# Kernel optimization log

Measured on AMD Instinct MI355X. Metric: run time of the kernel, lower is better.

Reference implementation:

```python
import jax, jax.numpy as jnp
import numpy as np

BATCH, INPUT_DIM, BOND_DIM, OUTPUT_DIM = 4096, 1024, 32, 512


def setup_inputs() -> dict:
    key = jax.random.key(0)
    k1, k2, k3 = jax.random.split(key, 3)
    # inputs centered at 1 so the length-1024 chain product stays O(1) in fp32
    inputs = 1.0 + 0.05 * jax.random.normal(k1, (BATCH, INPUT_DIM), dtype=jnp.float32)
    # cores scaled ~ glorot so each [bond,bond] step roughly preserves norm
    cores = jax.random.normal(k2, (INPUT_DIM, BOND_DIM, BOND_DIM), dtype=jnp.float32) / jnp.sqrt(jnp.float32(BOND_DIM))
    projection = jax.random.normal(k3, (BOND_DIM, OUTPUT_DIM), dtype=jnp.float32) * 0.05
    bias = jnp.zeros((OUTPUT_DIM,), dtype=jnp.float32)
    return {"inputs": inputs, "cores": cores, "projection": projection, "bias": bias}


def reference(inputs, cores, projection, bias):
    # MPS chain: boundary_{i+1}[b,k] = sum_j boundary_i[b,j] * x_i[b] * core_i[j,k]
    batch = inputs.shape[0]
    bond = cores.shape[1]
    boundary0 = jnp.ones((batch, bond), dtype=inputs.dtype)

    def step(boundary, xc):
        x_i, core_i = xc  # x_i: [batch], core_i: [bond, bond]
        new_boundary = (boundary * x_i[:, None]) @ core_i  # [batch, bond]
        return new_boundary, None

    xs = (inputs.T, cores)  # scan over input_dim axis
    final_boundary, _ = jax.lax.scan(step, boundary0, xs)
    return final_boundary @ projection + bias
```

## Files before the change

kernel.cpp:

```cpp
#include <hip/hip_runtime.h>


__device__ __forceinline__ void mm32(const float* __restrict__ A,
                                     const float* __restrict__ B,
                                     float* __restrict__ C, int tid) {
    const int j = tid >> 3;
    const int kq = tid & 7;
    float a[32];
    const float4* __restrict__ A4 = (const float4*)(A + j * 32);
#pragma unroll
    for (int t = 0; t < 8; ++t) {
        float4 v = A4[t];
        a[4 * t + 0] = v.x; a[4 * t + 1] = v.y;
        a[4 * t + 2] = v.z; a[4 * t + 3] = v.w;
    }
    const float4* __restrict__ B4 = (const float4*)B;
    float4 acc0 = make_float4(0.f, 0.f, 0.f, 0.f);
    float4 acc1 = make_float4(0.f, 0.f, 0.f, 0.f);
#pragma unroll
    for (int m = 0; m < 16; ++m) {
        float4 b0 = B4[m * 8 + kq];
        float4 b1 = B4[(m + 16) * 8 + kq];
        acc0.x = fmaf(a[m], b0.x, acc0.x);
        acc0.y = fmaf(a[m], b0.y, acc0.y);
        acc0.z = fmaf(a[m], b0.z, acc0.z);
        acc0.w = fmaf(a[m], b0.w, acc0.w);
        acc1.x = fmaf(a[m + 16], b1.x, acc1.x);
        acc1.y = fmaf(a[m + 16], b1.y, acc1.y);
        acc1.z = fmaf(a[m + 16], b1.z, acc1.z);
        acc1.w = fmaf(a[m + 16], b1.w, acc1.w);
    }
    float4 acc;
    acc.x = acc0.x + acc1.x; acc.y = acc0.y + acc1.y;
    acc.z = acc0.z + acc1.z; acc.w = acc0.w + acc1.w;
    ((float4*)(C + j * 32))[kq] = acc;
}

__global__ __launch_bounds__(256) void k1(const float* __restrict__ cores,
                                          const float* __restrict__ inputs,
                                          float* __restrict__ l1,
                                          float* __restrict__ p) {
    __shared__ __align__(16) float c[4 * 1024];
    __shared__ __align__(16) float ping[1024];
    __shared__ __align__(16) float pong[1024];
    const int tid = threadIdx.x;
    const int s = blockIdx.x;
    const int lane = tid & 63;
    const int wid = tid >> 6;

    const float4* src = (const float4*)(cores + (size_t)s * 4096);
    float4* cd = (float4*)c;
#pragma unroll
    for (int t = 0; t < 4; ++t) cd[tid + 256 * t] = src[tid + 256 * t];

    float prs[4];
#pragma unroll
    for (int rr = 0; rr < 4; ++rr) {
        const int row = s * 16 + wid * 4 + rr;
        const float4* in4 = (const float4*)(inputs + (size_t)row * 1024);
        float4 x0 = in4[lane];
        float4 x1 = in4[lane + 64];
        float4 x2 = in4[lane + 128];
        float4 x3 = in4[lane + 192];
        prs[rr] = ((x0.x * x0.y) * (x0.z * x0.w)) * ((x1.x * x1.y) * (x1.z * x1.w)) *
                  ((x2.x * x2.y) * (x2.z * x2.w)) * ((x3.x * x3.y) * (x3.z * x3.w));
    }
#pragma unroll
    for (int rr = 0; rr < 4; ++rr) {
        float pr = prs[rr];
#pragma unroll
        for (int msk = 1; msk < 64; msk <<= 1) pr *= __shfl_xor(pr, msk);
        if (lane == 0) p[s * 16 + wid * 4 + rr] = pr;
    }

    __syncthreads();
    mm32(c, c + 1024, ping, tid);
    __syncthreads();
    mm32(ping, c + 2048, pong, tid);
    __syncthreads();
    mm32(pong, c + 3072, ping, tid);
    __syncthreads();
    ((float4*)(l1 + (size_t)s * 1024))[tid] = ((const float4*)ping)[tid];
}

__global__ __launch_bounds__(256) void k2b(const float* __restrict__ l1,
                                           float* __restrict__ l2big) {
    __shared__ __align__(16) float m[16 * 1024];
    __shared__ __align__(16) float ping[1024];
    __shared__ __align__(16) float pong[1024];
    const int tid = threadIdx.x;
    const int s = blockIdx.x;
    const int seg = s & 15;
    const float4* src = (const float4*)(l1 + (size_t)seg * 16384);
    float4* md = (float4*)m;
#pragma unroll
    for (int t = 0; t < 16; ++t) md[tid + 256 * t] = src[tid + 256 * t];
    __syncthreads();
    mm32(m, m + 1024, ping, tid);
    __syncthreads();
    float* A = ping;
    float* C = pong;
    for (int t = 2; t < 16; ++t) {
        mm32(A, m + t * 1024, C, tid);
        __syncthreads();
        float* tmp = A; A = C; C = tmp;
    }
    ((float4*)(l2big + (size_t)s * 1024))[tid] = ((const float4*)A)[tid];
}

__global__ __launch_bounds__(256) void k4(const float* __restrict__ l2,
                                          const float* __restrict__ proj,
                                          const float* __restrict__ p,
                                          const float* __restrict__ bias,
                                          float* __restrict__ out) {
    __shared__ __align__(16) float M[16 * 1024];
    __shared__ __align__(16) float qL[512];
    __shared__ __align__(16) float bL[512];
    __shared__ float pL[16];
    __shared__ float w[32];
    const int tid = threadIdx.x;
    const int s = blockIdx.x;

    const float4* src = (const float4*)l2;
    float4* Md = (float4*)M;
#pragma unroll
    for (int t = 0; t < 16; ++t) Md[tid + 256 * t] = src[tid + 256 * t];
    if (tid < 128) ((float4*)bL)[tid] = ((const float4*)bias)[tid];
    if (tid < 16) pL[tid] = p[s * 16 + tid];
    __syncthreads();

    if (tid < 64) {
        const int k = tid & 31;
        float v = 1.0f;
        for (int sm = 0; sm < 16; ++sm) {
            const float* mat = M + sm * 1024 + k;
            float a0 = 0.f, a1 = 0.f, a2 = 0.f, a3 = 0.f;
#pragma unroll
            for (int j = 0; j < 8; ++j) {
                a0 = fmaf(__shfl(v, j),      mat[32 * j],        a0);
                a1 = fmaf(__shfl(v, j + 8),  mat[32 * (j + 8)],  a1);
                a2 = fmaf(__shfl(v, j + 16), mat[32 * (j + 16)], a2);
                a3 = fmaf(__shfl(v, j + 24), mat[32 * (j + 24)], a3);
            }
            v = (a0 + a1) + (a2 + a3);
        }
        if (tid < 32) w[k] = v;
    }
    __syncthreads();

    if (tid < 128) {
        const float4* P4 = (const float4*)proj;
        float4 acc = make_float4(0.f, 0.f, 0.f, 0.f);
#pragma unroll
        for (int j = 0; j < 32; ++j) {
            float wj = w[j];
            float4 pv = P4[j * 128 + tid];
            acc.x = fmaf(wj, pv.x, acc.x);
            acc.y = fmaf(wj, pv.y, acc.y);
            acc.z = fmaf(wj, pv.z, acc.z);
            acc.w = fmaf(wj, pv.w, acc.w);
        }
        ((float4*)qL)[tid] = acc;
    }
    __syncthreads();

    const float4* q4 = (const float4*)qL;
    const float4* b4 = (const float4*)bL;
#pragma unroll
    for (int rb = 0; rb < 2; ++rb) {
        const int r8 = rb * 8 + (tid >> 5);
        const int row = s * 16 + r8;
        const float pr = pL[r8];
        float4* o4 = (float4*)(out + (size_t)row * 512);
#pragma unroll
        for (int u = 0; u < 4; ++u) {
            const int c4 = u * 32 + (tid & 31);
            float4 qq = q4[c4];
            float4 bb = b4[c4];
            float4 r;
            r.x = fmaf(pr, qq.x, bb.x);
            r.y = fmaf(pr, qq.y, bb.y);
            r.z = fmaf(pr, qq.z, bb.z);
            r.w = fmaf(pr, qq.w, bb.w);
            o4[c4] = r;
        }
    }
}

extern "C" void kernel_launch(void* const* d_in, const int* in_sizes, int n_in,
                              void* d_out, int out_size, void* d_ws, size_t ws_size,
                              hipStream_t stream) {
    const float* inputs = (const float*)d_in[0];
    const float* cores  = (const float*)d_in[1];
    const float* proj   = (const float*)d_in[2];
    const float* bias   = (const float*)d_in[3];
    float* out = (float*)d_out;
    float* wsf = (float*)d_ws;
    float* l1    = wsf;
    float* l2big = wsf + 256 * 1024;
    float* p     = wsf + 512 * 1024;

    k1<<<256, 256, 0, stream>>>(cores, inputs, l1, p);
    k2b<<<256, 256, 0, stream>>>(l1, l2big);
    k4<<<256, 256, 0, stream>>>(l2big, proj, p, bias, out);
}
```

Before: 94.21 us.

## Fuse chain stages into two kernels with 16-core segments and double-buffered vector chain

```diff
diff --git a/kernel.cpp b/kernel.cpp
--- a/kernel.cpp
+++ b/kernel.cpp
@@ -36,22 +36,25 @@
     ((float4*)(C + j * 32))[kq] = acc;
 }
 
-__global__ __launch_bounds__(256) void k1(const float* __restrict__ cores,
-                                          const float* __restrict__ inputs,
-                                          float* __restrict__ l1,
-                                          float* __restrict__ p) {
-    __shared__ __align__(16) float c[4 * 1024];
+__global__ __launch_bounds__(256) void k1c(const float* __restrict__ cores,
+                                           const float* __restrict__ inputs,
+                                           float* __restrict__ l1p,
+                                           float* __restrict__ p) {
+    __shared__ __align__(16) float m[16 * 1024];
     __shared__ __align__(16) float ping[1024];
     __shared__ __align__(16) float pong[1024];
     const int tid = threadIdx.x;
     const int s = blockIdx.x;
     const int lane = tid & 63;
     const int wid = tid >> 6;
-
-    const float4* src = (const float4*)(cores + (size_t)s * 4096);
-    float4* cd = (float4*)c;
-#pragma unroll
-    for (int t = 0; t < 4; ++t) cd[tid + 256 * t] = src[tid + 256 * t];
+    const bool tree = (s < 64);
+
+    if (tree) {
+        const float4* src = (const float4*)(cores + (size_t)s * 16384);
+        float4* md = (float4*)m;
+#pragma unroll
+        for (int t = 0; t < 16; ++t) md[tid + 256 * t] = src[tid + 256 * t];
+    }
 
     float prs[4];
 #pragma unroll
@@ -73,28 +76,8 @@
         if (lane == 0) p[s * 16 + wid * 4 + rr] = pr;
     }
 
-    __syncthreads();
-    mm32(c, c + 1024, ping, tid);
-    __syncthreads();
-    mm32(ping, c + 2048, pong, tid);
-    __syncthreads();
-    mm32(pong, c + 3072, ping, tid);
-    __syncthreads();
-    ((float4*)(l1 + (size_t)s * 1024))[tid] = ((const float4*)ping)[tid];
-}
-
-__global__ __launch_bounds__(256) void k2b(const float* __restrict__ l1,
-                                           float* __restrict__ l2big) {
-    __shared__ __align__(16) float m[16 * 1024];
-    __shared__ __align__(16) float ping[1024];
-    __shared__ __align__(16) float pong[1024];
-    const int tid = threadIdx.x;
-    const int s = blockIdx.x;
-    const int seg = s & 15;
-    const float4* src = (const float4*)(l1 + (size_t)seg * 16384);
-    float4* md = (float4*)m;
-#pragma unroll
-    for (int t = 0; t < 16; ++t) md[tid + 256 * t] = src[tid + 256 * t];
+    if (!tree) return;
+
     __syncthreads();
     mm32(m, m + 1024, ping, tid);
     __syncthreads();
@@ -105,47 +88,61 @@
         __syncthreads();
         float* tmp = A; A = C; C = tmp;
     }
-    ((float4*)(l2big + (size_t)s * 1024))[tid] = ((const float4*)A)[tid];
-}
-
-__global__ __launch_bounds__(256) void k4(const float* __restrict__ l2,
-                                          const float* __restrict__ proj,
-                                          const float* __restrict__ p,
-                                          const float* __restrict__ bias,
-                                          float* __restrict__ out) {
-    __shared__ __align__(16) float M[16 * 1024];
+    ((float4*)(l1p + (size_t)s * 1024))[tid] = ((const float4*)A)[tid];
+}
+
+__global__ __launch_bounds__(256) void k4c(const float* __restrict__ l1p,
+                                           const float* __restrict__ proj,
+                                           const float* __restrict__ p,
+                                           const float* __restrict__ bias,
+                                           float* __restrict__ out) {
+    __shared__ __align__(16) float M[2][16 * 1024];
     __shared__ __align__(16) float qL[512];
     __shared__ __align__(16) float bL[512];
     __shared__ float pL[16];
     __shared__ float w[32];
     const int tid = threadIdx.x;
     const int s = blockIdx.x;
-
-    const float4* src = (const float4*)l2;
-    float4* Md = (float4*)M;
-#pragma unroll
-    for (int t = 0; t < 16; ++t) Md[tid + 256 * t] = src[tid + 256 * t];
+    const int k = tid & 31;
+
+    const float4* src = (const float4*)l1p;
+#pragma unroll
+    for (int t = 0; t < 16; ++t) ((float4*)M[0])[tid + 256 * t] = src[tid + 256 * t];
     if (tid < 128) ((float4*)bL)[tid] = ((const float4*)bias)[tid];
     if (tid < 16) pL[tid] = p[s * 16 + tid];
     __syncthreads();
 
-    if (tid < 64) {
-        const int k = tid & 31;
-        float v = 1.0f;
-        for (int sm = 0; sm < 16; ++sm) {
-            const float* mat = M + sm * 1024 + k;
-            float a0 = 0.f, a1 = 0.f, a2 = 0.f, a3 = 0.f;
-#pragma unroll
-            for (int j = 0; j < 8; ++j) {
-                a0 = fmaf(__shfl(v, j),      mat[32 * j],        a0);
-                a1 = fmaf(__shfl(v, j + 8),  mat[32 * (j + 8)],  a1);
-                a2 = fmaf(__shfl(v, j + 16), mat[32 * (j + 16)], a2);
-                a3 = fmaf(__shfl(v, j + 24), mat[32 * (j + 24)], a3);
+    float v = 1.0f;
+    for (int c = 0; c < 4; ++c) {
+        if (tid >= 64) {
+            if (c < 3) {
+                const float4* g = src + (c + 1) * 4096;
+                float4* d = (float4*)M[(c + 1) & 1];
+                const int base = tid - 64;
+#pragma unroll
+                for (int t = 0; t < 22; ++t) {
+                    const int i = base + 192 * t;
+                    if (i < 4096) d[i] = g[i];
+                }
             }
-            v = (a0 + a1) + (a2 + a3);
+        } else {
+            const float* Mc = M[c & 1];
+            for (int sm = 0; sm < 16; ++sm) {
+                const float* mat = Mc + sm * 1024 + k;
+                float a0 = 0.f, a1 = 0.f, a2 = 0.f, a3 = 0.f;
+#pragma unroll
+                for (int j = 0; j < 8; ++j) {
+                    a0 = fmaf(__shfl(v, j),      mat[32 * j],        a0);
+                    a1 = fmaf(__shfl(v, j + 8),  mat[32 * (j + 8)],  a1);
+                    a2 = fmaf(__shfl(v, j + 16), mat[32 * (j + 16)], a2);
+                    a3 = fmaf(__shfl(v, j + 24), mat[32 * (j + 24)], a3);
+                }
+                v = (a0 + a1) + (a2 + a3);
+            }
         }
-        if (tid < 32) w[k] = v;
-    }
+        __syncthreads();
+    }
+    if (tid < 32) w[k] = v;
     __syncthreads();
 
     if (tid < 128) {
@@ -196,11 +193,9 @@
     const float* bias   = (const float*)d_in[3];
     float* out = (float*)d_out;
     float* wsf = (float*)d_ws;
-    float* l1    = wsf;
-    float* l2big = wsf + 256 * 1024;
-    float* p     = wsf + 512 * 1024;
-
-    k1<<<256, 256, 0, stream>>>(cores, inputs, l1, p);
-    k2b<<<256, 256, 0, stream>>>(l1, l2big);
-    k4<<<256, 256, 0, stream>>>(l2big, proj, p, bias, out);
-}
+    float* l1p = wsf;
+    float* p   = wsf + 64 * 1024;
+
+    k1c<<<256, 256, 0, stream>>>(cores, inputs, l1p, p);
+    k4c<<<256, 256, 0, stream>>>(l1p, proj, p, bias, out);
+}
```

Result: slower. 103.2 us (+9.5%).
